# Kernel optimization log

Measured on AMD Instinct MI355X. Metric: run time of the kernel, lower is better.

The kernel has to match this reference:

```python
import jax, jax.numpy as jnp
import numpy as np

N = 50000      # nodes
E = 1600000    # edges (before self loops)
B = 512        # graphs
D = 128        # gcn dim (constant across the 3 GAT layers)
H = 1024       # hidden_dim
O = 128        # output_dim
NEG_SLOPE = 0.2


def setup_inputs() -> dict:
    key = jax.random.key(0)
    ks = jax.random.split(key, 24)
    inp = {
        "x": jax.random.normal(ks[0], (N, D), jnp.float32),
        "edge_index": jax.random.randint(ks[1], (2, E), 0, N, dtype=jnp.int64),
        "edge_weight": jax.random.uniform(ks[2], (E,), jnp.float32),
        "batch": jnp.sort(jax.random.randint(ks[3], (N,), 0, B, dtype=jnp.int64)),
    }
    s = 1.0 / np.sqrt(D)
    for i in range(3):
        k = 4 + 4 * i
        inp[f"W{i+1}"] = jax.random.normal(ks[k], (D, D), jnp.float32) * s
        inp[f"as{i+1}"] = jax.random.normal(ks[k + 1], (D,), jnp.float32) * s
        inp[f"ad{i+1}"] = jax.random.normal(ks[k + 2], (D,), jnp.float32) * s
        inp[f"b{i+1}"] = jnp.zeros((D,), jnp.float32)
    inp["Wf1"] = jax.random.normal(ks[16], (D, H), jnp.float32) * s
    inp["bf1"] = jnp.zeros((H,), jnp.float32)
    inp["Wf2"] = jax.random.normal(ks[17], (H, O), jnp.float32) * (1.0 / np.sqrt(H))
    inp["bf2"] = jnp.zeros((O,), jnp.float32)
    return inp


def gat_conv(x, src, dst, W, a_src, a_dst, b):
    """PyG GATConv, heads=1: gather -> leakyrelu -> segment softmax -> scatter-add."""
    h = x @ W                                   # [N, D]
    e = jax.nn.leaky_relu(jnp.take(h @ a_src, src) + jnp.take(h @ a_dst, dst), NEG_SLOPE)  # [E']
    m = jax.ops.segment_max(e, dst, num_segments=N)
    ex = jnp.exp(e - m[dst])
    denom = jax.ops.segment_sum(ex, dst, num_segments=N)
    alpha = ex / denom[dst]                      # segment softmax over incoming edges
    out = jax.ops.segment_sum(alpha[:, None] * h[src], dst, num_segments=N)
    return out + b


def reference(x, edge_index, edge_weight, batch,
              W1, as1, ad1, b1, W2, as2, ad2, b2, W3, as3, ad3, b3,
              Wf1, bf1, Wf2, bf2):
    # GATConv adds self loops; edge_weight is unused by GATConv (faithful to original)
    loop = jnp.arange(N, dtype=edge_index.dtype)
    src = jnp.concatenate([edge_index[0], loop])
    dst = jnp.concatenate([edge_index[1], loop])

    h = gat_conv(x, src, dst, W1, as1, ad1, b1)
    h = jax.nn.relu(gat_conv(h, src, dst, W2, as2, ad2, b2))
    h = jax.nn.relu(gat_conv(h, src, dst, W3, as3, ad3, b3))

    # global mean pool (gep)
    sums = jax.ops.segment_sum(h, batch, num_segments=B)        # [B, D]
    counts = jax.ops.segment_sum(jnp.ones((N,), h.dtype), batch, num_segments=B)
    pooled = sums / jnp.maximum(counts, 1.0)[:, None]

    # MLP head; dropout is identity at inference
    o = jax.nn.relu(pooled) @ Wf1 + bf1
    o = jax.nn.relu(o) @ Wf2 + bf2
    return o
```

## Files before the change

### kernel.cpp

```cpp
#include <hip/hip_runtime.h>
#include <cstdint>
#include <cstddef>

#define NEG_SLOPE 0.2f

typedef _Float16 f16x8 __attribute__((ext_vector_type(8)));
typedef float f32x4v __attribute__((ext_vector_type(4)));

__device__ __forceinline__ unsigned enc_f(float f) {
  unsigned u = __float_as_uint(f);
  return (u & 0x80000000u) ? ~u : (u | 0x80000000u);
}
__device__ __forceinline__ float dec_f(unsigned u) {
  return (u & 0x80000000u) ? __uint_as_float(u ^ 0x80000000u) : __uint_as_float(~u);
}
__device__ __forceinline__ unsigned short f2bf(float f) {
  unsigned u = __float_as_uint(f);
  unsigned r = u + 0x7fffu + ((u >> 16) & 1u);
  return (unsigned short)(r >> 16);
}
#define BLO(u) __uint_as_float((u) << 16)
#define BHI(u) __uint_as_float((u) & 0xffff0000u)

__global__ void k_init(int* counts, unsigned* maxPart, int N) {
  int n = blockIdx.x * blockDim.x + threadIdx.x;
  if (n < N) counts[n] = 1;
  if (n < 768) maxPart[n] = 0u;
}

__global__ void k_count_rank(const int* __restrict__ dst, int E,
                             int* counts, int* __restrict__ rank) {
  int i = (blockIdx.x * blockDim.x + threadIdx.x) * 4;
  if (i + 3 < E) {
    int4 d = *(const int4*)&dst[i];
    int4 r;
    r.x = atomicAdd(&counts[d.x], 1);
    r.y = atomicAdd(&counts[d.y], 1);
    r.z = atomicAdd(&counts[d.z], 1);
    r.w = atomicAdd(&counts[d.w], 1);
    *(int4*)&rank[i] = r;
  } else {
    for (int e = i; e < E; e++) rank[e] = atomicAdd(&counts[dst[e]], 1);
  }
}
__global__ void k_count_rank_s(const int* __restrict__ dst, int E,
                               int* counts, int* __restrict__ rank) {
  int e = blockIdx.x * blockDim.x + threadIdx.x;
  if (e < E) rank[e] = atomicAdd(&counts[dst[e]], 1);
}

__global__ __launch_bounds__(1024) void k_scan1(const int* __restrict__ counts, int N,
                                                int* __restrict__ row_ptr, int* __restrict__ part) {
  __shared__ int tmp[1024];
  int t = threadIdx.x;
  int i = blockIdx.x * 1024 + t;
  int v = (i < N) ? counts[i] : 0;
  tmp[t] = v;
  __syncthreads();
  for (int off = 1; off < 1024; off <<= 1) {
    int u = (t >= off) ? tmp[t - off] : 0;
    __syncthreads();
    tmp[t] += u;
    __syncthreads();
  }
  if (i < N) row_ptr[i + 1] = tmp[t];
  if (t == 1023) part[blockIdx.x] = tmp[t];
}

__global__ void k_scan2(int* part, int nb, int* row_ptr) {
  if (threadIdx.x == 0 && blockIdx.x == 0) {
    int run = 0;
    for (int b = 0; b < nb; b++) { int v = part[b]; part[b] = run; run += v; }
    row_ptr[0] = 0;
  }
}

__global__ __launch_bounds__(1024) void k_scan3(int* __restrict__ row_ptr,
                                                const int* __restrict__ part, int N) {
  int i = blockIdx.x * 1024 + threadIdx.x;
  if (i < N) row_ptr[i + 1] += part[blockIdx.x];
}

__global__ void k_fill_self(const int* __restrict__ row_ptr, int* __restrict__ col, int N) {
  int n = blockIdx.x * blockDim.x + threadIdx.x;
  if (n < N) col[row_ptr[n]] = n;
}

__global__ void k_fill(const int* __restrict__ src, const int* __restrict__ dst,
                       const int* __restrict__ rank, int E,
                       const int* __restrict__ row_ptr, int* __restrict__ col) {
  int i = (blockIdx.x * blockDim.x + threadIdx.x) * 4;
  if (i + 3 < E) {
    int4 s = *(const int4*)&src[i];
    int4 d = *(const int4*)&dst[i];
    int4 r = *(const int4*)&rank[i];
    col[row_ptr[d.x] + r.x] = s.x;
    col[row_ptr[d.y] + r.y] = s.y;
    col[row_ptr[d.z] + r.z] = s.z;
    col[row_ptr[d.w] + r.w] = s.w;
  } else {
    for (int e = i; e < E; e++) col[row_ptr[dst[e]] + rank[e]] = src[e];
  }
}
__global__ void k_fill_s(const int* __restrict__ src, const int* __restrict__ dst,
                         const int* __restrict__ rank, int E,
                         const int* __restrict__ row_ptr, int* __restrict__ col) {
  int e = blockIdx.x * blockDim.x + threadIdx.x;
  if (e < E) col[row_ptr[dst[e]] + rank[e]] = src[e];
}

#define AST 136
#define WST 136
#define HST 132
__global__ __launch_bounds__(256) void k_gemm_fused(const float* __restrict__ A,
                                                    const float* __restrict__ W,
                                                    unsigned short* __restrict__ hb,
                                                    const float* __restrict__ asrc,
                                                    const float* __restrict__ adst,
                                                    float* __restrict__ sv, float* __restrict__ dv,
                                                    unsigned* __restrict__ maxSlot, int M) {
  __shared__ __align__(16) char smem[64 * AST * 2 + 128 * WST * 2];
  _Float16* Ah = (_Float16*)smem;
  _Float16* Wt = (_Float16*)(smem + 64 * AST * 2);
  float*    hS = (float*)(smem + 64 * AST * 2);
  __shared__ float redmax[4];
  int t = threadIdx.x;
  int rowbase = blockIdx.x * 64;

  for (int i = t; i < 64 * 32; i += 256) {
    int r = i >> 5, c4 = (i & 31) << 2;
    int gr = rowbase + r;
    float4 v = make_float4(0.f, 0.f, 0.f, 0.f);
    if (gr < M) v = *(const float4*)&A[(size_t)gr * 128 + c4];
    _Float16 tmp[4] = {(_Float16)v.x, (_Float16)v.y, (_Float16)v.z, (_Float16)v.w};
    *(short4*)&Ah[r * AST + c4] = *(short4*)tmp;
  }
  for (int i = t; i < 128 * 32; i += 256) {
    int r = i >> 5, c4 = (i & 31) << 2;
    float4 v = *(const float4*)&W[(size_t)r * 128 + c4];
    Wt[(c4 + 0) * WST + r] = (_Float16)v.x;
    Wt[(c4 + 1) * WST + r] = (_Float16)v.y;
    Wt[(c4 + 2) * WST + r] = (_Float16)v.z;
    Wt[(c4 + 3) * WST + r] = (_Float16)v.w;
  }
  __syncthreads();

  int wave = t >> 6, lane = t & 63, quad = lane >> 4, l15 = lane & 15;
  f32x4v acc[4][2];
#pragma unroll
  for (int mt = 0; mt < 4; mt++)
#pragma unroll
    for (int nt = 0; nt < 2; nt++) {
      acc[mt][nt][0] = 0.f; acc[mt][nt][1] = 0.f; acc[mt][nt][2] = 0.f; acc[mt][nt][3] = 0.f;
    }

#pragma unroll
  for (int s = 0; s < 4; s++) {
    int k0 = (s << 5) + (quad << 3);
    f16x8 af[4], bf[2];
#pragma unroll
    for (int mt = 0; mt < 4; mt++)
      af[mt] = *(f16x8*)&Ah[(mt * 16 + l15) * AST + k0];
#pragma unroll
    for (int nt = 0; nt < 2; nt++)
      bf[nt] = *(f16x8*)&Wt[(wave * 32 + nt * 16 + l15) * WST + k0];
#pragma unroll
    for (int mt = 0; mt < 4; mt++)
#pragma unroll
      for (int nt = 0; nt < 2; nt++)
        acc[mt][nt] = __builtin_amdgcn_mfma_f32_16x16x32_f16(af[mt], bf[nt], acc[mt][nt], 0, 0, 0);
  }
  __syncthreads();

#pragma unroll
  for (int mt = 0; mt < 4; mt++)
#pragma unroll
    for (int nt = 0; nt < 2; nt++)
#pragma unroll
      for (int rr = 0; rr < 4; rr++)
        hS[(mt * 16 + quad * 4 + rr) * HST + wave * 32 + nt * 16 + l15] = acc[mt][nt][rr];
  __syncthreads();

  int tx = t & 31, ty = t >> 5;
  float4 av  = *(const float4*)&asrc[tx * 4];
  float4 adv = *(const float4*)&adst[tx * 4];
  float wmax = -1e30f;
#pragma unroll
  for (int r8 = 0; r8 < 8; r8++) {
    int row = r8 * 8 + ty;
    int gr = rowbase + row;
    float4 hv = *(float4*)&hS[row * HST + tx * 4];
    float ps = hv.x * av.x + hv.y * av.y + hv.z * av.z + hv.w * av.w;
    float pd = hv.x * adv.x + hv.y * adv.y + hv.z * adv.z + hv.w * adv.w;
#pragma unroll
    for (int mask = 16; mask; mask >>= 1) {
      ps += __shfl_xor(ps, mask);
      pd += __shfl_xor(pd, mask);
    }
    if (gr < M) {
      ushort4 hq;
      hq.x = f2bf(hv.x); hq.y = f2bf(hv.y); hq.z = f2bf(hv.z); hq.w = f2bf(hv.w);
      *(ushort4*)&hb[(size_t)gr * 128 + tx * 4] = hq;
      if (tx == 0) { sv[gr] = ps; dv[gr] = pd; wmax = fmaxf(wmax, ps); }
    }
  }
#pragma unroll
  for (int mask = 32; mask; mask >>= 1) wmax = fmaxf(wmax, __shfl_xor(wmax, mask));
  if ((t & 63) == 0) redmax[t >> 6] = wmax;
  __syncthreads();
  if (t == 0) {
    float mx = fmaxf(fmaxf(redmax[0], redmax[1]), fmaxf(redmax[2], redmax[3]));
    atomicMax(&maxSlot[blockIdx.x & 255], enc_f(mx));
  }
}

__global__ __launch_bounds__(256) void k_agg(const unsigned short* __restrict__ hb,
                                             const float* __restrict__ sv,
                                             const float* __restrict__ dv,
                                             const int* __restrict__ row_ptr,
                                             const int* __restrict__ col,
                                             const float* __restrict__ bias,
                                             const unsigned* __restrict__ maxSlot,
                                             float* __restrict__ out, int N, int relu) {
  int wid = (int)((blockIdx.x * (size_t)blockDim.x + threadIdx.x) >> 6);
  int lane = threadIdx.x & 63;
  if (wid >= N) return;

  unsigned mp = max(max(maxSlot[lane], maxSlot[lane + 64]),
                    max(maxSlot[lane + 128], maxSlot[lane + 192]));
#pragma unroll
  for (int off = 32; off; off >>= 1) mp = max(mp, __shfl_xor(mp, off));
  float maxS = dec_f(mp);

  int beg = row_ptr[wid], end = row_ptr[wid + 1];
  float dn = dv[wid];
  float m = maxS + dn;
  m = (m > 0.f) ? m : NEG_SLOPE * m;

  int g = lane >> 4, sub = lane & 15;
  const uint32_t* hbu = (const uint32_t*)hb;
  float acc[8];
#pragma unroll
  for (int k = 0; k < 8; k++) acc[k] = 0.f;
  float dsum = 0.f;

  for (int j = beg + g; j < end; j += 4) {
    int sn = col[j];
    float e = sv[sn] + dn;
    e = (e > 0.f) ? e : NEG_SLOPE * e;
    float wgt = __expf(e - m);
    dsum += wgt;
    uint4 hv = *(const uint4*)(hbu + (size_t)sn * 64 + sub * 4);
    acc[0] += wgt * BLO(hv.x); acc[1] += wgt * BHI(hv.x);
    acc[2] += wgt * BLO(hv.y); acc[3] += wgt * BHI(hv.y);
    acc[4] += wgt * BLO(hv.z); acc[5] += wgt * BHI(hv.z);
    acc[6] += wgt * BLO(hv.w); acc[7] += wgt * BHI(hv.w);
  }
  dsum += __shfl_xor(dsum, 16);
  dsum += __shfl_xor(dsum, 32);
#pragma unroll
  for (int k = 0; k < 8; k++) {
    acc[k] += __shfl_xor(acc[k], 16);
    acc[k] += __shfl_xor(acc[k], 32);
  }
  if (lane < 16) {
    float inv = 1.f / dsum;
    float4 b0 = *(const float4*)&bias[sub * 8];
    float4 b1 = *(const float4*)&bias[sub * 8 + 4];
    float4 o0, o1;
    o0.x = acc[0] * inv + b0.x; o0.y = acc[1] * inv + b0.y;
    o0.z = acc[2] * inv + b0.z; o0.w = acc[3] * inv + b0.w;
    o1.x = acc[4] * inv + b1.x; o1.y = acc[5] * inv + b1.y;
    o1.z = acc[6] * inv + b1.z; o1.w = acc[7] * inv + b1.w;
    if (relu) {
      o0.x = fmaxf(o0.x, 0.f); o0.y = fmaxf(o0.y, 0.f); o0.z = fmaxf(o0.z, 0.f); o0.w = fmaxf(o0.w, 0.f);
      o1.x = fmaxf(o1.x, 0.f); o1.y = fmaxf(o1.y, 0.f); o1.z = fmaxf(o1.z, 0.f); o1.w = fmaxf(o1.w, 0.f);
    }
    float* op = &out[(size_t)wid * 128 + sub * 8];
    *(float4*)op = o0;
    *(float4*)(op + 4) = o1;
  }
}

__global__ void k_bounds(const int* __restrict__ batch, int N, int B, int* __restrict__ gstart) {
  int n = blockIdx.x * blockDim.x + threadIdx.x;
  if (n >= N) return;
  int cur = batch[n];
  if (n == 0) {
    for (int g = 0; g <= cur; g++) gstart[g] = 0;
  } else {
    int prev = batch[n - 1];
    for (int g = prev + 1; g <= cur; g++) gstart[g] = n;
  }
  if (n == N - 1) {
    for (int g = cur + 1; g <= B; g++) gstart[g] = N;
  }
}

__global__ __launch_bounds__(128) void k_pool(const float* __restrict__ h,
                                              const int* __restrict__ gstart,
                                              float* __restrict__ pooled, int B) {
  int b = blockIdx.x, c = threadIdx.x;
  int s0 = gstart[b], s1 = gstart[b + 1];
  float acc = 0.f;
  for (int n = s0; n < s1; n++) acc += h[(size_t)n * 128 + c];
  int cnt = s1 - s0;
  float p = acc / (float)(cnt > 0 ? cnt : 1);
  pooled[b * 128 + c] = fmaxf(p, 0.f);
}

__global__ __launch_bounds__(256) void k_mlp(const float* __restrict__ pooled,
                                             const float* __restrict__ Wf1,
                                             const float* __restrict__ bf1,
                                             const float* __restrict__ Wf2,
                                             const float* __restrict__ bf2,
                                             float* __restrict__ out, int B) {
  __shared__ float P[4][128];
  __shared__ float H1[4][1024];
  __shared__ float R[4][128];
  int t = threadIdx.x;
  int g0 = blockIdx.x * 4;

  for (int i = t; i < 4 * 128; i += 256) {
    int gi = i >> 7, c = i & 127;
    P[gi][c] = (g0 + gi < B) ? pooled[(size_t)(g0 + gi) * 128 + c] : 0.f;
  }
  __syncthreads();

#pragma unroll
  for (int cb = 0; cb < 4; cb++) {
    int c = cb * 256 + t;
    float a0 = 0.f, a1 = 0.f, a2 = 0.f, a3 = 0.f;
    for (int k = 0; k < 128; k++) {
      float w = Wf1[(size_t)k * 1024 + c];
      a0 += P[0][k] * w; a1 += P[1][k] * w; a2 += P[2][k] * w; a3 += P[3][k] * w;
    }
    float b = bf1[c];
    H1[0][c] = fmaxf(a0 + b, 0.f);
    H1[1][c] = fmaxf(a1 + b, 0.f);
    H1[2][c] = fmaxf(a2 + b, 0.f);
    H1[3][c] = fmaxf(a3 + b, 0.f);
  }
  __syncthreads();

  int c = t & 127, hh = t >> 7;
  float a0 = 0.f, a1 = 0.f, a2 = 0.f, a3 = 0.f;
  int k0 = hh * 512;
  for (int k = k0; k < k0 + 512; k++) {
    float w = Wf2[(size_t)k * 128 + c];
    a0 += H1[0][k] * w; a1 += H1[1][k] * w; a2 += H1[2][k] * w; a3 += H1[3][k] * w;
  }
  if (hh == 1) { R[0][c] = a0; R[1][c] = a1; R[2][c] = a2; R[3][c] = a3; }
  __syncthreads();
  if (hh == 0) {
    float b = bf2[c];
    float o0 = a0 + R[0][c] + b;
    float o1 = a1 + R[1][c] + b;
    float o2 = a2 + R[2][c] + b;
    float o3 = a3 + R[3][c] + b;
    if (g0 + 0 < B) out[(size_t)(g0 + 0) * 128 + c] = o0;
    if (g0 + 1 < B) out[(size_t)(g0 + 1) * 128 + c] = o1;
    if (g0 + 2 < B) out[(size_t)(g0 + 2) * 128 + c] = o2;
    if (g0 + 3 < B) out[(size_t)(g0 + 3) * 128 + c] = o3;
  }
}

extern "C" void kernel_launch(void* const* d_in, const int* in_sizes, int n_in,
                              void* d_out, int out_size, void* d_ws, size_t ws_size,
                              hipStream_t stream) {
  const float* x     = (const float*)d_in[0];
  const int*   ei    = (const int*)d_in[1];
  const int*   batch = (const int*)d_in[3];
  const float* W1 = (const float*)d_in[4];
  const float* as1 = (const float*)d_in[5];
  const float* ad1 = (const float*)d_in[6];
  const float* b1 = (const float*)d_in[7];
  const float* W2 = (const float*)d_in[8];
  const float* as2 = (const float*)d_in[9];
  const float* ad2 = (const float*)d_in[10];
  const float* b2 = (const float*)d_in[11];
  const float* W3 = (const float*)d_in[12];
  const float* as3 = (const float*)d_in[13];
  const float* ad3 = (const float*)d_in[14];
  const float* b3 = (const float*)d_in[15];
  const float* Wf1 = (const float*)d_in[16];
  const float* bf1 = (const float*)d_in[17];
  const float* Wf2 = (const float*)d_in[18];
  const float* bf2 = (const float*)d_in[19];

  const int N = in_sizes[0] / 128;
  const int E = in_sizes[1] / 2;
  const int B = out_size / 128;

  char* base = (char*)d_ws;
  size_t off = 0;
  auto carve = [&](size_t bytes) -> void* {
    off = (off + 255) & ~(size_t)255;
    void* p = base + off;
    off += bytes;
    return p;
  };
  int* counts   = (int*)carve((size_t)N * 4);
  int* row_ptr  = (int*)carve((size_t)(N + 1) * 4);
  int* rank     = (int*)carve((size_t)E * 4);
  int* col      = (int*)carve((size_t)(E + N) * 4);
  int* part     = (int*)carve(1024 * 4);
  int* gstart   = (int*)carve((size_t)(B + 1) * 4);
  unsigned* maxPart = (unsigned*)carve(768 * 4);
  float* sbuf   = (float*)carve((size_t)N * 4);
  float* dbuf   = (float*)carve((size_t)N * 4);
  unsigned short* hb = (unsigned short*)carve((size_t)N * 128 * 2);
  float* abuf   = (float*)carve((size_t)N * 128 * 4);
  float* pooled = (float*)carve((size_t)B * 128 * 4);

  const int* srcp = ei;
  const int* dstp = ei + E;
  const int nb = (N + 1023) / 1024;

  hipLaunchKernelGGL(k_init, dim3((N + 255) / 256), dim3(256), 0, stream, counts, maxPart, N);
  if ((E & 3) == 0) {
    int nq = E / 4;
    hipLaunchKernelGGL(k_count_rank, dim3((nq + 255) / 256), dim3(256), 0, stream, dstp, E, counts, rank);
  } else {
    hipLaunchKernelGGL(k_count_rank_s, dim3((E + 255) / 256), dim3(256), 0, stream, dstp, E, counts, rank);
  }
  hipLaunchKernelGGL(k_scan1, dim3(nb), dim3(1024), 0, stream, counts, N, row_ptr, part);
  hipLaunchKernelGGL(k_scan2, dim3(1), dim3(64), 0, stream, part, nb, row_ptr);
  hipLaunchKernelGGL(k_scan3, dim3(nb), dim3(1024), 0, stream, row_ptr, part, N);
  hipLaunchKernelGGL(k_fill_self, dim3((N + 255) / 256), dim3(256), 0, stream, row_ptr, col, N);
  if ((E & 3) == 0) {
    int nq = E / 4;
    hipLaunchKernelGGL(k_fill, dim3((nq + 255) / 256), dim3(256), 0, stream, srcp, dstp, rank, E, row_ptr, col);
  } else {
    hipLaunchKernelGGL(k_fill_s, dim3((E + 255) / 256), dim3(256), 0, stream, srcp, dstp, rank, E, row_ptr, col);
  }
  hipLaunchKernelGGL(k_bounds, dim3((N + 255) / 256), dim3(256), 0, stream, batch, N, B, gstart);

  const float* Wl[3] = {W1, W2, W3};
  const float* al[3] = {as1, as2, as3};
  const float* dl[3] = {ad1, ad2, ad3};
  const float* bl[3] = {b1, b2, b3};
  const float* cur = x;
  for (int L = 0; L < 3; L++) {
    hipLaunchKernelGGL(k_gemm_fused, dim3((N + 63) / 64), dim3(256), 0, stream,
                       cur, Wl[L], hb, al[L], dl[L], sbuf, dbuf, maxPart + L * 256, N);
    hipLaunchKernelGGL(k_agg, dim3((N + 3) / 4), dim3(256), 0, stream,
                       hb, sbuf, dbuf, row_ptr, col, bl[L], maxPart + L * 256, abuf, N, (L > 0) ? 1 : 0);
    cur = abuf;
  }

  hipLaunchKernelGGL(k_pool, dim3(B), dim3(128), 0, stream, abuf, gstart, pooled, B);
  hipLaunchKernelGGL(k_mlp, dim3((B + 3) / 4), dim3(256), 0, stream,
                     pooled, Wf1, bf1, Wf2, bf2, (float*)d_out, B);
}
```

Measured before the change: 580.6 us.

## Privatize CSR counters, fuse edge counting with layer-1 GEMM, unroll aggregation

Edge degree counting now uses 8 privatized counter arrays selected by edge chunk, which spreads atomic contention, and a new k_base kernel computes per-partition bases for the fill. The counting blocks are merged into the same launch as the first layer's GEMM, so the two independent jobs run concurrently and one launch is saved. The aggregation loop handles two neighbors per iteration to expose more memory-level parallelism. In exchange it uses more workspace, adds an 8-way read in the scan, and the fused launch allocates GEMM-sized shared memory for every block, including the counting ones.

```diff
diff --git a/kernel.cpp b/kernel.cpp
--- a/kernel.cpp
+++ b/kernel.cpp
@@ -22,96 +22,153 @@
 #define BLO(u) __uint_as_float((u) << 16)
 #define BHI(u) __uint_as_float((u) & 0xffff0000u)
 
-__global__ void k_init(int* counts, unsigned* maxPart, int N) {
-  int n = blockIdx.x * blockDim.x + threadIdx.x;
-  if (n < N) counts[n] = 1;
-  if (n < 768) maxPart[n] = 0u;
-}
-
-__global__ void k_count_rank(const int* __restrict__ dst, int E,
-                             int* counts, int* __restrict__ rank) {
-  int i = (blockIdx.x * blockDim.x + threadIdx.x) * 4;
-  if (i + 3 < E) {
-    int4 d = *(const int4*)&dst[i];
-    int4 r;
-    r.x = atomicAdd(&counts[d.x], 1);
-    r.y = atomicAdd(&counts[d.y], 1);
-    r.z = atomicAdd(&counts[d.z], 1);
-    r.w = atomicAdd(&counts[d.w], 1);
-    *(int4*)&rank[i] = r;
-  } else {
-    for (int e = i; e < E; e++) rank[e] = atomicAdd(&counts[dst[e]], 1);
-  }
-}
-__global__ void k_count_rank_s(const int* __restrict__ dst, int E,
-                               int* counts, int* __restrict__ rank) {
-  int e = blockIdx.x * blockDim.x + threadIdx.x;
-  if (e < E) rank[e] = atomicAdd(&counts[dst[e]], 1);
-}
-
-__global__ __launch_bounds__(1024) void k_scan1(const int* __restrict__ counts, int N,
-                                                int* __restrict__ row_ptr, int* __restrict__ part) {
-  __shared__ int tmp[1024];
-  int t = threadIdx.x;
-  int i = blockIdx.x * 1024 + t;
-  int v = (i < N) ? counts[i] : 0;
-  tmp[t] = v;
-  __syncthreads();
-  for (int off = 1; off < 1024; off <<= 1) {
-    int u = (t >= off) ? tmp[t - off] : 0;
-    __syncthreads();
-    tmp[t] += u;
-    __syncthreads();
-  }
-  if (i < N) row_ptr[i + 1] = tmp[t];
-  if (t == 1023) part[blockIdx.x] = tmp[t];
-}
-
-__global__ void k_scan2(int* part, int nb, int* row_ptr) {
-  if (threadIdx.x == 0 && blockIdx.x == 0) {
-    int run = 0;
-    for (int b = 0; b < nb; b++) { int v = part[b]; part[b] = run; run += v; }
-    row_ptr[0] = 0;
-  }
-}
-
-__global__ __launch_bounds__(1024) void k_scan3(int* __restrict__ row_ptr,
-                                                const int* __restrict__ part, int N) {
-  int i = blockIdx.x * 1024 + threadIdx.x;
-  if (i < N) row_ptr[i + 1] += part[blockIdx.x];
-}
-
-__global__ void k_fill_self(const int* __restrict__ row_ptr, int* __restrict__ col, int N) {
-  int n = blockIdx.x * blockDim.x + threadIdx.x;
-  if (n < N) col[row_ptr[n]] = n;
-}
-
-__global__ void k_fill(const int* __restrict__ src, const int* __restrict__ dst,
-                       const int* __restrict__ rank, int E,
-                       const int* __restrict__ row_ptr, int* __restrict__ col) {
-  int i = (blockIdx.x * blockDim.x + threadIdx.x) * 4;
-  if (i + 3 < E) {
-    int4 s = *(const int4*)&src[i];
-    int4 d = *(const int4*)&dst[i];
-    int4 r = *(const int4*)&rank[i];
-    col[row_ptr[d.x] + r.x] = s.x;
-    col[row_ptr[d.y] + r.y] = s.y;
-    col[row_ptr[d.z] + r.z] = s.z;
-    col[row_ptr[d.w] + r.w] = s.w;
-  } else {
-    for (int e = i; e < E; e++) col[row_ptr[dst[e]] + rank[e]] = src[e];
-  }
-}
-__global__ void k_fill_s(const int* __restrict__ src, const int* __restrict__ dst,
-                         const int* __restrict__ rank, int E,
-                         const int* __restrict__ row_ptr, int* __restrict__ col) {
-  int e = blockIdx.x * blockDim.x + threadIdx.x;
-  if (e < E) col[row_ptr[dst[e]] + rank[e]] = src[e];
-}
-
 #define AST 136
 #define WST 136
 #define HST 132
+#define SMEM_BYTES (64 * AST * 2 + 128 * WST * 2)
+
+__global__ void k_init(int* c, unsigned* maxPart, int N8) {
+  int n = blockIdx.x * blockDim.x + threadIdx.x;
+  if (n < N8) c[n] = 0;
+  if (n < 768) maxPart[n] = 0u;
+}
+
+__device__ __forceinline__ void gemm_body(char* smem, float* redmax, int bx,
+                                          const float* __restrict__ A,
+                                          const float* __restrict__ W,
+                                          unsigned short* __restrict__ hb,
+                                          const float* __restrict__ asrc,
+                                          const float* __restrict__ adst,
+                                          float* __restrict__ sv, float* __restrict__ dv,
+                                          unsigned* __restrict__ maxSlot, int M) {
+  _Float16* Ah = (_Float16*)smem;
+  _Float16* Wt = (_Float16*)(smem + 64 * AST * 2);
+  float*    hS = (float*)(smem + 64 * AST * 2);
+  int t = threadIdx.x;
+  int rowbase = bx * 64;
+
+  for (int i = t; i < 64 * 32; i += 256) {
+    int r = i >> 5, c4 = (i & 31) << 2;
+    int gr = rowbase + r;
+    float4 v = make_float4(0.f, 0.f, 0.f, 0.f);
+    if (gr < M) v = *(const float4*)&A[(size_t)gr * 128 + c4];
+    _Float16 tmp[4] = {(_Float16)v.x, (_Float16)v.y, (_Float16)v.z, (_Float16)v.w};
+    *(short4*)&Ah[r * AST + c4] = *(short4*)tmp;
+  }
+  for (int i = t; i < 128 * 32; i += 256) {
+    int r = i >> 5, c4 = (i & 31) << 2;
+    float4 v = *(const float4*)&W[(size_t)r * 128 + c4];
+    Wt[(c4 + 0) * WST + r] = (_Float16)v.x;
+    Wt[(c4 + 1) * WST + r] = (_Float16)v.y;
+    Wt[(c4 + 2) * WST + r] = (_Float16)v.z;
+    Wt[(c4 + 3) * WST + r] = (_Float16)v.w;
+  }
+  __syncthreads();
+
+  int wave = t >> 6, lane = t & 63, quad = lane >> 4, l15 = lane & 15;
+  f32x4v acc[4][2];
+#pragma unroll
+  for (int mt = 0; mt < 4; mt++)
+#pragma unroll
+    for (int nt = 0; nt < 2; nt++) {
+      acc[mt][nt][0] = 0.f; acc[mt][nt][1] = 0.f; acc[mt][nt][2] = 0.f; acc[mt][nt][3] = 0.f;
+    }
+
+#pragma unroll
+  for (int s = 0; s < 4; s++) {
+    int k0 = (s << 5) + (quad << 3);
+    f16x8 af[4], bf[2];
+#pragma unroll
+    for (int mt = 0; mt < 4; mt++)
+      af[mt] = *(f16x8*)&Ah[(mt * 16 + l15) * AST + k0];
+#pragma unroll
+    for (int nt = 0; nt < 2; nt++)
+      bf[nt] = *(f16x8*)&Wt[(wave * 32 + nt * 16 + l15) * WST + k0];
+#pragma unroll
+    for (int mt = 0; mt < 4; mt++)
+#pragma unroll
+      for (int nt = 0; nt < 2; nt++)
+        acc[mt][nt] = __builtin_amdgcn_mfma_f32_16x16x32_f16(af[mt], bf[nt], acc[mt][nt], 0, 0, 0);
+  }
+  __syncthreads();
+
+#pragma unroll
+  for (int mt = 0; mt < 4; mt++)
+#pragma unroll
+    for (int nt = 0; nt < 2; nt++)
+#pragma unroll
+      for (int rr = 0; rr < 4; rr++)
+        hS[(mt * 16 + quad * 4 + rr) * HST + wave * 32 + nt * 16 + l15] = acc[mt][nt][rr];
+  __syncthreads();
+
+  int tx = t & 31, ty = t >> 5;
+  float4 av  = *(const float4*)&asrc[tx * 4];
+  float4 adv = *(const float4*)&adst[tx * 4];
+  float wmax = -1e30f;
+#pragma unroll
+  for (int r8 = 0; r8 < 8; r8++) {
+    int row = r8 * 8 + ty;
+    int gr = rowbase + row;
+    float4 hv = *(float4*)&hS[row * HST + tx * 4];
+    float ps = hv.x * av.x + hv.y * av.y + hv.z * av.z + hv.w * av.w;
+    float pd = hv.x * adv.x + hv.y * adv.y + hv.z * adv.z + hv.w * adv.w;
+#pragma unroll
+    for (int mask = 16; mask; mask >>= 1) {
+      ps += __shfl_xor(ps, mask);
+      pd += __shfl_xor(pd, mask);
+    }
+    if (gr < M) {
+      ushort4 hq;
+      hq.x = f2bf(hv.x); hq.y = f2bf(hv.y); hq.z = f2bf(hv.z); hq.w = f2bf(hv.w);
+      *(ushort4*)&hb[(size_t)gr * 128 + tx * 4] = hq;
+      if (tx == 0) { sv[gr] = ps; dv[gr] = pd; wmax = fmaxf(wmax, ps); }
+    }
+  }
+#pragma unroll
+  for (int mask = 32; mask; mask >>= 1) wmax = fmaxf(wmax, __shfl_xor(wmax, mask));
+  if ((t & 63) == 0) redmax[t >> 6] = wmax;
+  __syncthreads();
+  if (t == 0) {
+    float mx = fmaxf(fmaxf(redmax[0], redmax[1]), fmaxf(redmax[2], redmax[3]));
+    atomicMax(&maxSlot[blockIdx.x & 255], enc_f(mx));
+  }
+}
+
+__global__ __launch_bounds__(256) void k_mega1(const float* __restrict__ A,
+                                               const float* __restrict__ W,
+                                               unsigned short* __restrict__ hb,
+                                               const float* __restrict__ asrc,
+                                               const float* __restrict__ adst,
+                                               float* __restrict__ sv, float* __restrict__ dv,
+                                               unsigned* __restrict__ maxSlot, int M,
+                                               const int* __restrict__ dst, int E,
+                                               int* c, int* __restrict__ rank,
+                                               int Gc, int vec4) {
+  __shared__ __align__(16) char smem[SMEM_BYTES];
+  __shared__ float redmax[4];
+  if ((int)blockIdx.x < Gc) {
+    int i = (blockIdx.x << 10) + threadIdx.x * 4;
+    if (vec4 && i + 3 < E) {
+      int p = (i >> 10) & 7;
+      int* cp = c + (size_t)p * M;
+      int4 d = *(const int4*)&dst[i];
+      int4 r;
+      r.x = atomicAdd(&cp[d.x], 1);
+      r.y = atomicAdd(&cp[d.y], 1);
+      r.z = atomicAdd(&cp[d.z], 1);
+      r.w = atomicAdd(&cp[d.w], 1);
+      *(int4*)&rank[i] = r;
+    } else {
+      for (int e = i; e < min(i + 4, E); e++) {
+        int p = (e >> 10) & 7;
+        rank[e] = atomicAdd(&c[(size_t)p * M + dst[e]], 1);
+      }
+    }
+  } else {
+    gemm_body(smem, redmax, (int)blockIdx.x - Gc, A, W, hb, asrc, adst, sv, dv, maxSlot, M);
+  }
+}
+
 __global__ __launch_bounds__(256) void k_gemm_fused(const float* __restrict__ A,
                                                     const float* __restrict__ W,
                                                     unsigned short* __restrict__ hb,
@@ -119,98 +176,81 @@
                                                     const float* __restrict__ adst,
                                                     float* __restrict__ sv, float* __restrict__ dv,
                                                     unsigned* __restrict__ maxSlot, int M) {
-  __shared__ __align__(16) char smem[64 * AST * 2 + 128 * WST * 2];
-  _Float16* Ah = (_Float16*)smem;
-  _Float16* Wt = (_Float16*)(smem + 64 * AST * 2);
-  float*    hS = (float*)(smem + 64 * AST * 2);
+  __shared__ __align__(16) char smem[SMEM_BYTES];
   __shared__ float redmax[4];
+  gemm_body(smem, redmax, (int)blockIdx.x, A, W, hb, asrc, adst, sv, dv, maxSlot, M);
+}
+
+__global__ __launch_bounds__(1024) void k_scan1(const int* __restrict__ c, int N,
+                                                int* __restrict__ row_ptr, int* __restrict__ part) {
+  __shared__ int tmp[1024];
   int t = threadIdx.x;
-  int rowbase = blockIdx.x * 64;
-
-  for (int i = t; i < 64 * 32; i += 256) {
-    int r = i >> 5, c4 = (i & 31) << 2;
-    int gr = rowbase + r;
-    float4 v = make_float4(0.f, 0.f, 0.f, 0.f);
-    if (gr < M) v = *(const float4*)&A[(size_t)gr * 128 + c4];
-    _Float16 tmp[4] = {(_Float16)v.x, (_Float16)v.y, (_Float16)v.z, (_Float16)v.w};
-    *(short4*)&Ah[r * AST + c4] = *(short4*)tmp;
-  }
-  for (int i = t; i < 128 * 32; i += 256) {
-    int r = i >> 5, c4 = (i & 31) << 2;
-    float4 v = *(const float4*)&W[(size_t)r * 128 + c4];
-    Wt[(c4 + 0) * WST + r] = (_Float16)v.x;
-    Wt[(c4 + 1) * WST + r] = (_Float16)v.y;
-    Wt[(c4 + 2) * WST + r] = (_Float16)v.z;
-    Wt[(c4 + 3) * WST + r] = (_Float16)v.w;
-  }
-  __syncthreads();
-
-  int wave = t >> 6, lane = t & 63, quad = lane >> 4, l15 = lane & 15;
-  f32x4v acc[4][2];
-#pragma unroll
-  for (int mt = 0; mt < 4; mt++)
-#pragma unroll
-    for (int nt = 0; nt < 2; nt++) {
-      acc[mt][nt][0] = 0.f; acc[mt][nt][1] = 0.f; acc[mt][nt][2] = 0.f; acc[mt][nt][3] = 0.f;
-    }
-
-#pragma unroll
-  for (int s = 0; s < 4; s++) {
-    int k0 = (s << 5) + (quad << 3);
-    f16x8 af[4], bf[2];
-#pragma unroll
-    for (int mt = 0; mt < 4; mt++)
-      af[mt] = *(f16x8*)&Ah[(mt * 16 + l15) * AST + k0];
-#pragma unroll
-    for (int nt = 0; nt < 2; nt++)
-      bf[nt] = *(f16x8*)&Wt[(wave * 32 + nt * 16 + l15) * WST + k0];
-#pragma unroll
-    for (int mt = 0; mt < 4; mt++)
-#pragma unroll
-      for (int nt = 0; nt < 2; nt++)
-        acc[mt][nt] = __builtin_amdgcn_mfma_f32_16x16x32_f16(af[mt], bf[nt], acc[mt][nt], 0, 0, 0);
-  }
-  __syncthreads();
-
-#pragma unroll
-  for (int mt = 0; mt < 4; mt++)
-#pragma unroll
-    for (int nt = 0; nt < 2; nt++)
-#pragma unroll
-      for (int rr = 0; rr < 4; rr++)
-        hS[(mt * 16 + quad * 4 + rr) * HST + wave * 32 + nt * 16 + l15] = acc[mt][nt][rr];
-  __syncthreads();
-
-  int tx = t & 31, ty = t >> 5;
-  float4 av  = *(const float4*)&asrc[tx * 4];
-  float4 adv = *(const float4*)&adst[tx * 4];
-  float wmax = -1e30f;
-#pragma unroll
-  for (int r8 = 0; r8 < 8; r8++) {
-    int row = r8 * 8 + ty;
-    int gr = rowbase + row;
-    float4 hv = *(float4*)&hS[row * HST + tx * 4];
-    float ps = hv.x * av.x + hv.y * av.y + hv.z * av.z + hv.w * av.w;
-    float pd = hv.x * adv.x + hv.y * adv.y + hv.z * adv.z + hv.w * adv.w;
-#pragma unroll
-    for (int mask = 16; mask; mask >>= 1) {
-      ps += __shfl_xor(ps, mask);
-      pd += __shfl_xor(pd, mask);
-    }
-    if (gr < M) {
-      ushort4 hq;
-      hq.x = f2bf(hv.x); hq.y = f2bf(hv.y); hq.z = f2bf(hv.z); hq.w = f2bf(hv.w);
-      *(ushort4*)&hb[(size_t)gr * 128 + tx * 4] = hq;
-      if (tx == 0) { sv[gr] = ps; dv[gr] = pd; wmax = fmaxf(wmax, ps); }
-    }
-  }
-#pragma unroll
-  for (int mask = 32; mask; mask >>= 1) wmax = fmaxf(wmax, __shfl_xor(wmax, mask));
-  if ((t & 63) == 0) redmax[t >> 6] = wmax;
-  __syncthreads();
-  if (t == 0) {
-    float mx = fmaxf(fmaxf(redmax[0], redmax[1]), fmaxf(redmax[2], redmax[3]));
-    atomicMax(&maxSlot[blockIdx.x & 255], enc_f(mx));
+  int i = blockIdx.x * 1024 + t;
+  int v = 0;
+  if (i < N) {
+    v = 1;
+#pragma unroll
+    for (int p = 0; p < 8; p++) v += c[(size_t)p * N + i];
+  }
+  tmp[t] = v;
+  __syncthreads();
+  for (int off = 1; off < 1024; off <<= 1) {
+    int u = (t >= off) ? tmp[t - off] : 0;
+    __syncthreads();
+    tmp[t] += u;
+    __syncthreads();
+  }
+  if (i < N) row_ptr[i + 1] = tmp[t];
+  if (t == 1023) part[blockIdx.x] = tmp[t];
+}
+
+__global__ void k_scan2(int* part, int nb, int* row_ptr) {
+  if (threadIdx.x == 0 && blockIdx.x == 0) {
+    int run = 0;
+    for (int b = 0; b < nb; b++) { int v = part[b]; part[b] = run; run += v; }
+    row_ptr[0] = 0;
+  }
+}
+
+__global__ __launch_bounds__(1024) void k_scan3(int* __restrict__ row_ptr,
+                                                const int* __restrict__ part, int N) {
+  int i = blockIdx.x * 1024 + threadIdx.x;
+  if (i < N) row_ptr[i + 1] += part[blockIdx.x];
+}
+
+__global__ void k_base(const int* __restrict__ row_ptr, const int* __restrict__ c,
+                       int* __restrict__ base, int* __restrict__ col, int N) {
+  int n = blockIdx.x * blockDim.x + threadIdx.x;
+  if (n >= N) return;
+  int b = row_ptr[n];
+  col[b] = n;
+  b++;
+#pragma unroll
+  for (int p = 0; p < 8; p++) {
+    base[(size_t)p * N + n] = b;
+    b += c[(size_t)p * N + n];
+  }
+}
+
+__global__ void k_fill(const int* __restrict__ src, const int* __restrict__ dst,
+                       const int* __restrict__ rank, int E, int N,
+                       const int* __restrict__ base, int* __restrict__ col, int vec4) {
+  int i = (blockIdx.x * blockDim.x + threadIdx.x) * 4;
+  if (vec4 && i + 3 < E) {
+    int p = (i >> 10) & 7;
+    const int* bp = base + (size_t)p * N;
+    int4 s = *(const int4*)&src[i];
+    int4 d = *(const int4*)&dst[i];
+    int4 r = *(const int4*)&rank[i];
+    col[bp[d.x] + r.x] = s.x;
+    col[bp[d.y] + r.y] = s.y;
+    col[bp[d.z] + r.z] = s.z;
+    col[bp[d.w] + r.w] = s.w;
+  } else {
+    for (int e = i; e < min(i + 4, E); e++) {
+      int p = (e >> 10) & 7;
+      col[base[(size_t)p * N + dst[e]] + rank[e]] = src[e];
+    }
   }
 }
 
@@ -244,7 +284,29 @@
   for (int k = 0; k < 8; k++) acc[k] = 0.f;
   float dsum = 0.f;
 
-  for (int j = beg + g; j < end; j += 4) {
+  int j = beg + g;
+  for (; j + 4 < end; j += 8) {
+    int sn0 = col[j];
+    int sn1 = col[j + 4];
+    float e0 = sv[sn0] + dn;
+    float e1 = sv[sn1] + dn;
+    e0 = (e0 > 0.f) ? e0 : NEG_SLOPE * e0;
+    e1 = (e1 > 0.f) ? e1 : NEG_SLOPE * e1;
+    float w0 = __expf(e0 - m);
+    float w1 = __expf(e1 - m);
+    dsum += w0 + w1;
+    uint4 h0 = *(const uint4*)(hbu + (size_t)sn0 * 64 + sub * 4);
+    uint4 h1 = *(const uint4*)(hbu + (size_t)sn1 * 64 + sub * 4);
+    acc[0] += w0 * BLO(h0.x) + w1 * BLO(h1.x);
+    acc[1] += w0 * BHI(h0.x) + w1 * BHI(h1.x);
+    acc[2] += w0 * BLO(h0.y) + w1 * BLO(h1.y);
+    acc[3] += w0 * BHI(h0.y) + w1 * BHI(h1.y);
+    acc[4] += w0 * BLO(h0.z) + w1 * BLO(h1.z);
+    acc[5] += w0 * BHI(h0.z) + w1 * BHI(h1.z);
+    acc[6] += w0 * BLO(h0.w) + w1 * BLO(h1.w);
+    acc[7] += w0 * BHI(h0.w) + w1 * BHI(h1.w);
+  }
+  if (j < end) {
     int sn = col[j];
     float e = sv[sn] + dn;
     e = (e > 0.f) ? e : NEG_SLOPE * e;
@@ -392,15 +454,16 @@
   const int E = in_sizes[1] / 2;
   const int B = out_size / 128;
 
-  char* base = (char*)d_ws;
+  char* base_ws = (char*)d_ws;
   size_t off = 0;
   auto carve = [&](size_t bytes) -> void* {
     off = (off + 255) & ~(size_t)255;
-    void* p = base + off;
+    void* p = base_ws + off;
     off += bytes;
     return p;
   };
-  int* counts   = (int*)carve((size_t)N * 4);
+  int* c        = (int*)carve((size_t)8 * N * 4);
+  int* base     = (int*)carve((size_t)8 * N * 4);
   int* row_ptr  = (int*)carve((size_t)(N + 1) * 4);
   int* rank     = (int*)carve((size_t)E * 4);
   int* col      = (int*)carve((size_t)(E + N) * 4);
@@ -416,37 +479,37 @@
   const int* srcp = ei;
   const int* dstp = ei + E;
   const int nb = (N + 1023) / 1024;
-
-  hipLaunchKernelGGL(k_init, dim3((N + 255) / 256), dim3(256), 0, stream, counts, maxPart, N);
-  if ((E & 3) == 0) {
-    int nq = E / 4;
-    hipLaunchKernelGGL(k_count_rank, dim3((nq + 255) / 256), dim3(256), 0, stream, dstp, E, counts, rank);
-  } else {
-    hipLaunchKernelGGL(k_count_rank_s, dim3((E + 255) / 256), dim3(256), 0, stream, dstp, E, counts, rank);
-  }
-  hipLaunchKernelGGL(k_scan1, dim3(nb), dim3(1024), 0, stream, counts, N, row_ptr, part);
+  const int Gc = (E + 1023) >> 10;
+  const int Gg = (N + 63) / 64;
+  const int vec4 = ((E & 3) == 0) ? 1 : 0;
+
+  hipLaunchKernelGGL(k_init, dim3((8 * N + 255) / 256), dim3(256), 0, stream, c, maxPart, 8 * N);
+  hipLaunchKernelGGL(k_bounds, dim3((N + 255) / 256), dim3(256), 0, stream, batch, N, B, gstart);
+
+  hipLaunchKernelGGL(k_mega1, dim3(Gc + Gg), dim3(256), 0, stream,
+                     x, W1, hb, as1, ad1, sbuf, dbuf, maxPart + 0 * 256, N,
+                     dstp, E, c, rank, Gc, vec4);
+
+  hipLaunchKernelGGL(k_scan1, dim3(nb), dim3(1024), 0, stream, c, N, row_ptr, part);
   hipLaunchKernelGGL(k_scan2, dim3(1), dim3(64), 0, stream, part, nb, row_ptr);
   hipLaunchKernelGGL(k_scan3, dim3(nb), dim3(1024), 0, stream, row_ptr, part, N);
-  hipLaunchKernelGGL(k_fill_self, dim3((N + 255) / 256), dim3(256), 0, stream, row_ptr, col, N);
-  if ((E & 3) == 0) {
-    int nq = E / 4;
-    hipLaunchKernelGGL(k_fill, dim3((nq + 255) / 256), dim3(256), 0, stream, srcp, dstp, rank, E, row_ptr, col);
-  } else {
-    hipLaunchKernelGGL(k_fill_s, dim3((E + 255) / 256), dim3(256), 0, stream, srcp, dstp, rank, E, row_ptr, col);
-  }
-  hipLaunchKernelGGL(k_bounds, dim3((N + 255) / 256), dim3(256), 0, stream, batch, N, B, gstart);
+  hipLaunchKernelGGL(k_base, dim3((N + 255) / 256), dim3(256), 0, stream, row_ptr, c, base, col, N);
+  hipLaunchKernelGGL(k_fill, dim3((E + 1023) / 1024), dim3(256), 0, stream,
+                     srcp, dstp, rank, E, N, base, col, vec4);
+
+  hipLaunchKernelGGL(k_agg, dim3((N + 3) / 4), dim3(256), 0, stream,
+                     hb, sbuf, dbuf, row_ptr, col, b1, maxPart + 0 * 256, abuf, N, 0);
 
   const float* Wl[3] = {W1, W2, W3};
   const float* al[3] = {as1, as2, as3};
   const float* dl[3] = {ad1, ad2, ad3};
-  const float* bl[3] = {b1, b2, b3};
-  const float* cur = x;
-  for (int L = 0; L < 3; L++) {
+  const float* bl[3] = {b2, b3, b3};
+  for (int L = 1; L < 3; L++) {
+    const float* Ws = Wl[L];
     hipLaunchKernelGGL(k_gemm_fused, dim3((N + 63) / 64), dim3(256), 0, stream,
-                       cur, Wl[L], hb, al[L], dl[L], sbuf, dbuf, maxPart + L * 256, N);
+                       abuf, Ws, hb, al[L], dl[L], sbuf, dbuf, maxPart + L * 256, N);
     hipLaunchKernelGGL(k_agg, dim3((N + 3) / 4), dim3(256), 0, stream,
-                       hb, sbuf, dbuf, row_ptr, col, bl[L], maxPart + L * 256, abuf, N, (L > 0) ? 1 : 0);
-    cur = abuf;
+                       hb, sbuf, dbuf, row_ptr, col, (L == 1) ? b2 : b3, maxPart + L * 256, abuf, N, 1);
   }
 
   hipLaunchKernelGGL(k_pool, dim3(B), dim3(128), 0, stream, abuf, gstart, pooled, B);
```

Result: faster. 555.1 us (-4.4%).
